# Kernel tuning notes

Measured on AMD Instinct MI355X. Metric: run time of the kernel, lower is better.

Reference implementation:

```python
import jax, jax.numpy as jnp
import numpy as np

T, B, IN_S, H, OUT_S = 2048, 4096, 1, 20, 1


def setup_inputs() -> dict:
    key = jax.random.key(0)
    k_u, k_ih, k_hh, k_out = jax.random.split(key, 4)
    s = 1.0 / np.sqrt(H)  # PyTorch-style uniform init scale (values only; math identical)
    return {
        "u": jax.random.normal(k_u, (T, B, IN_S), dtype=jnp.float32),
        "W_ih": jax.random.uniform(k_ih, (4 * H, IN_S), minval=-s, maxval=s, dtype=jnp.float32),
        "W_hh": jax.random.uniform(k_hh, (4 * H, H), minval=-s, maxval=s, dtype=jnp.float32),
        "W_out": jax.random.uniform(k_out, (OUT_S, H), minval=-s, maxval=s, dtype=jnp.float32),
    }


def _lstm(u, W_ih, W_hh):
    # u: [T, B, IN_S]; PyTorch gate order: i, f, g, o. No biases (bias=False).
    Tn, Bn, _ = u.shape
    # Precompute input projections for all timesteps at once: [T, B, 4H]
    x_proj = jnp.einsum("tbi,gi->tbg", u, W_ih)

    def step(carry, xg):
        h, c = carry  # [B, H] each
        gates = xg + h @ W_hh.T  # [B, 4H]
        i, f, g, o = jnp.split(gates, 4, axis=-1)
        i = jax.nn.sigmoid(i)
        f = jax.nn.sigmoid(f)
        g = jnp.tanh(g)
        o = jax.nn.sigmoid(o)
        c = f * c + i * g
        h = o * jnp.tanh(c)
        return (h, c), h

    h0 = jnp.zeros((Bn, W_hh.shape[1]), dtype=u.dtype)
    c0 = jnp.zeros_like(h0)
    (_, _), ys = jax.lax.scan(step, (h0, c0), x_proj)
    return ys  # [T, B, H]


def reference(u, W_ih, W_hh, W_out):
    ys = _lstm(u, W_ih, W_hh)          # [T, B, H]
    return jnp.einsum("tbh,oh->tbo", ys, W_out)  # [T, B, OUT_S]
```

## Files before the change

### kernel.cpp

```cpp
#include <hip/hip_runtime.h>
#include <hip/hip_bf16.h>
#include <math.h>

#define TT 2048
#define BB 4096
#define HH 20

typedef float v2f __attribute__((ext_vector_type(2)));

#define L2E 1.4426950408889634f

__device__ __forceinline__ float rcp_fast(float x)  { return __builtin_amdgcn_rcpf(x); }
__device__ __forceinline__ float exp2_fast(float x) { return __builtin_amdgcn_exp2f(x); }

__device__ __forceinline__ v2f pk_fma(v2f a, v2f b, v2f c) {
    return __builtin_elementwise_fma(a, b, c);
}
__device__ __forceinline__ v2f exp2v(v2f x) { v2f r; r.x = exp2_fast(x.x); r.y = exp2_fast(x.y); return r; }
__device__ __forceinline__ v2f rcpv(v2f x)  { v2f r; r.x = rcp_fast(x.x);  r.y = rcp_fast(x.y);  return r; }
__device__ __forceinline__ v2f absv(v2f x)  { v2f r; r.x = fabsf(x.x);     r.y = fabsf(x.y);     return r; }
__device__ __forceinline__ v2f csignv(v2f x, v2f s) {
    v2f r; r.x = copysignf(x.x, s.x); r.y = copysignf(x.y, s.y); return r;
}

__global__ __launch_bounds__(64, 1) void lstm_fused_kernel(
    const float* __restrict__ u,
    const float* __restrict__ W_ih,
    const float* __restrict__ W_hh,
    const float* __restrict__ W_out,
    float* __restrict__ y)
{
    __shared__ __align__(16) float hbuf[128];

    const int lane = threadIdx.x;
    int q, wa, jbase;
    bool is_y = false;
    if (lane < 40) {
        q = lane / 10;
        const int p = lane - q * 10;
        wa = q * HH + 2 * p;
        jbase = 2 * p;
    } else {
        is_y = (lane < 44);
        q = is_y ? (lane - 40) : 0;
        wa = 4 * HH + (lane - 40) * 2;
        jbase = 0;
    }

    for (int i = lane; i < 128; i += 64) hbuf[i] = 0.0f;
    asm volatile("" ::: "memory");

    v2f wgv[4][2][10];
    v2f wihv[4][2];
    const float gsc[4] = {-L2E, -L2E, -2.0f * L2E, -L2E};
    #pragma unroll
    for (int g = 0; g < 4; ++g) {
        #pragma unroll
        for (int r = 0; r < 2; ++r) {
            const int row = g * HH + jbase + r;
            #pragma unroll
            for (int m = 0; m < 10; ++m) {
                wgv[g][r][m].x = gsc[g] * W_hh[row * HH + 2 * m];
                wgv[g][r][m].y = gsc[g] * W_hh[row * HH + 2 * m + 1];
            }
            wihv[g][r].x = gsc[g] * W_ih[row];
            wihv[g][r].y = 0.0f;
        }
    }
    if (lane >= 40) {
        #pragma unroll
        for (int m = 0; m < 10; ++m) {
            wgv[0][0][m].x = W_out[2 * m];
            wgv[0][0][m].y = W_out[2 * m + 1];
        }
        wihv[0][0].x = 0.0f;
    }

    const v2f* hs = (const v2f*)&hbuf[q * HH];
    v2f* hw = (v2f*)&hbuf[wa];

    v2f cv = {0.0f, 0.0f};
    const float* __restrict__ up = u + (size_t)blockIdx.x * 4 + q;
    float* yp = y + (size_t)blockIdx.x * 4 + (lane - 40);

    float u_cur[8];
    #pragma unroll
    for (int k = 0; k < 8; ++k) u_cur[k] = up[(size_t)k * BB];

    const v2f one = {1.0f, 1.0f};
    const v2f n2l2e = {-2.0f * L2E, -2.0f * L2E};

    for (int t8 = 0; t8 < TT; t8 += 8) {
        #pragma unroll
        for (int g = 0; g < 4; ++g) {
            #pragma unroll
            for (int r = 0; r < 2; ++r) {
                #pragma unroll
                for (int m = 0; m < 10; ++m)
                    asm volatile("" : "+v"(wgv[g][r][m].x), "+v"(wgv[g][r][m].y));
                asm volatile("" : "+v"(wihv[g][r].x));
            }
        }

        const int tn = (t8 + 8 < TT) ? (t8 + 8) : t8;
        float u_nxt[8];
        #pragma unroll
        for (int k = 0; k < 8; ++k) u_nxt[k] = up[(size_t)(tn + k) * BB];

        float y8[8];

        #pragma unroll
        for (int tt = 0; tt < 8; ++tt) {
            v2f h2[10];
            #pragma unroll
            for (int m = 0; m < 10; ++m) h2[m] = hs[m];

            const float uv = u_cur[tt];
            const v2f uv2 = {uv, uv};
            v2f a[4][2];
            #pragma unroll
            for (int g = 0; g < 4; ++g) {
                #pragma unroll
                for (int r = 0; r < 2; ++r) a[g][r] = wihv[g][r] * uv2;
            }

            #pragma unroll
            for (int m = 0; m < 10; ++m) {
                const v2f hp = h2[m];
                a[2][0] = pk_fma(wgv[2][0][m], hp, a[2][0]);
                a[2][1] = pk_fma(wgv[2][1][m], hp, a[2][1]);
                a[1][0] = pk_fma(wgv[1][0][m], hp, a[1][0]);
                a[1][1] = pk_fma(wgv[1][1][m], hp, a[1][1]);
                a[0][0] = pk_fma(wgv[0][0][m], hp, a[0][0]);
                a[0][1] = pk_fma(wgv[0][1][m], hp, a[0][1]);
                a[3][0] = pk_fma(wgv[3][0][m], hp, a[3][0]);
                a[3][1] = pk_fma(wgv[3][1][m], hp, a[3][1]);
            }
            v2f gi, gf, gg, go;
            gi.x = a[0][0].x + a[0][0].y;  gi.y = a[0][1].x + a[0][1].y;
            gf.x = a[1][0].x + a[1][0].y;  gf.y = a[1][1].x + a[1][1].y;
            gg.x = a[2][0].x + a[2][0].y;  gg.y = a[2][1].x + a[2][1].y;
            go.x = a[3][0].x + a[3][0].y;  go.y = a[3][1].x + a[3][1].y;
            y8[tt] = gi.x;

            const v2f eg = exp2v(gg);
            const v2f ef = exp2v(gf);
            const v2f ei = exp2v(gi);
            const v2f eo = exp2v(go);
            const v2f pg = one + eg, pf = one + ef, pi2 = one + ei, po = one + eo;
            const v2f mg = one - eg;

            const v2f m1  = pg * pi2;
            const v2f num = pk_fma(cv, m1, mg * pf);
            const v2f rv  = rcpv(pf * m1);
            cv = num * rv;
            const v2f kn  = absv(num) * n2l2e;
            const v2f ec  = exp2v(kn * rv);
            const v2f pc  = one + ec;
            const v2f mcs = csignv(one - ec, num);
            const v2f hv  = mcs * rcpv(po * pc);

            *hw = hv;
        }

        if (is_y) {
            #pragma unroll
            for (int k = 0; k < 8; ++k) {
                const int idx = t8 - 1 + k;
                if (idx >= 0) yp[(size_t)idx * BB] = y8[k];
            }
        }

        #pragma unroll
        for (int k = 0; k < 8; ++k) u_cur[k] = u_nxt[k];
    }

    {
        v2f ay = {0.0f, 0.0f};
        #pragma unroll
        for (int m = 0; m < 10; ++m) ay = pk_fma(wgv[0][0][m], hs[m], ay);
        if (is_y) yp[(size_t)(TT - 1) * BB] = ay.x + ay.y;
    }
}

extern "C" void kernel_launch(void* const* d_in, const int* in_sizes, int n_in,
                              void* d_out, int out_size, void* d_ws, size_t ws_size,
                              hipStream_t stream) {
    const float* u     = (const float*)d_in[0];
    const float* W_ih  = (const float*)d_in[1];
    const float* W_hh  = (const float*)d_in[2];
    const float* W_out = (const float*)d_in[3];
    float* y = (float*)d_out;

    const int blocks = BB / 4;
    lstm_fused_kernel<<<dim3(blocks), dim3(64), 0, stream>>>(u, W_ih, W_hh, W_out, y);
}
```

Before: 742.6 us.

## Interleave two independent batch groups per wavefront to hide recurrence latency

Each 64-lane block now advances two independent groups of four batch elements (A and B) through the same timesteps, using the shared register-resident weights. The grid is halved to compensate. The goal is to hide the latency of the serial chain (LDS read, FMA, exp, reciprocal) by giving the scheduler a second independent chain to interleave within one wave. In exchange, half as many waves occupy the GPU's SIMDs, each wave needs more registers for the extra accumulators and hidden-state copies, and the unroll depth per load batch drops from 8 to 4 timesteps. The asm register-pinning barriers are also removed.

```diff
diff --git a/kernel.cpp b/kernel.cpp
--- a/kernel.cpp
+++ b/kernel.cpp
@@ -30,24 +30,27 @@
     const float* __restrict__ W_out,
     float* __restrict__ y)
 {
-    __shared__ __align__(16) float hbuf[128];
+    __shared__ __align__(16) float hbuf[224];
 
     const int lane = threadIdx.x;
-    int q, wa, jbase;
-    bool is_y = false;
+    int q = 0, jbase = 0, waA, waB;
+    bool is_yA = false, is_yB = false;
     if (lane < 40) {
         q = lane / 10;
         const int p = lane - q * 10;
-        wa = q * HH + 2 * p;
         jbase = 2 * p;
+        waA = q * HH + 2 * p;
+        waB = 80 + q * HH + 2 * p;
     } else {
-        is_y = (lane < 44);
-        q = is_y ? (lane - 40) : 0;
-        wa = 4 * HH + (lane - 40) * 2;
-        jbase = 0;
-    }
-
-    for (int i = lane; i < 128; i += 64) hbuf[i] = 0.0f;
+        is_yA = (lane < 44);
+        is_yB = (lane >= 44) && (lane < 48);
+        waA = 160 + (lane - 40) * 2;
+        waB = 160 + (lane - 40) * 2;
+    }
+    const int rbA = is_yA ? (lane - 40) * HH : (lane < 40 ? q * HH : 0);
+    const int rbB = 80 + (is_yB ? (lane - 44) * HH : (lane < 40 ? q * HH : 0));
+
+    for (int i = lane; i < 224; i += 64) hbuf[i] = 0.0f;
     asm volatile("" ::: "memory");
 
     v2f wgv[4][2][10];
@@ -76,110 +79,165 @@
         wihv[0][0].x = 0.0f;
     }
 
-    const v2f* hs = (const v2f*)&hbuf[q * HH];
-    v2f* hw = (v2f*)&hbuf[wa];
-
-    v2f cv = {0.0f, 0.0f};
-    const float* __restrict__ up = u + (size_t)blockIdx.x * 4 + q;
-    float* yp = y + (size_t)blockIdx.x * 4 + (lane - 40);
-
-    float u_cur[8];
+    const v2f* hsA = (const v2f*)&hbuf[rbA];
+    const v2f* hsB = (const v2f*)&hbuf[rbB];
+    v2f* hwA = (v2f*)&hbuf[waA];
+    v2f* hwB = (v2f*)&hbuf[waB];
+
+    v2f cvA = {0.0f, 0.0f}, cvB = {0.0f, 0.0f};
+    const size_t base = (size_t)blockIdx.x * 8;
+    const float* upA = u + base + (lane < 40 ? q : 0);
+    const float* upB = u + base + 4 + (lane < 40 ? q : 0);
+    float* ypA = y + base + (lane - 40);
+    float* ypB = y + base + 4 + (lane - 44);
+
+    float u_curA[4], u_curB[4];
     #pragma unroll
-    for (int k = 0; k < 8; ++k) u_cur[k] = up[(size_t)k * BB];
+    for (int k = 0; k < 4; ++k) { u_curA[k] = upA[(size_t)k * BB]; u_curB[k] = upB[(size_t)k * BB]; }
 
     const v2f one = {1.0f, 1.0f};
     const v2f n2l2e = {-2.0f * L2E, -2.0f * L2E};
 
-    for (int t8 = 0; t8 < TT; t8 += 8) {
-        #pragma unroll
-        for (int g = 0; g < 4; ++g) {
-            #pragma unroll
-            for (int r = 0; r < 2; ++r) {
-                #pragma unroll
-                for (int m = 0; m < 10; ++m)
-                    asm volatile("" : "+v"(wgv[g][r][m].x), "+v"(wgv[g][r][m].y));
-                asm volatile("" : "+v"(wihv[g][r].x));
-            }
-        }
-
-        const int tn = (t8 + 8 < TT) ? (t8 + 8) : t8;
-        float u_nxt[8];
-        #pragma unroll
-        for (int k = 0; k < 8; ++k) u_nxt[k] = up[(size_t)(tn + k) * BB];
-
-        float y8[8];
-
-        #pragma unroll
-        for (int tt = 0; tt < 8; ++tt) {
-            v2f h2[10];
-            #pragma unroll
-            for (int m = 0; m < 10; ++m) h2[m] = hs[m];
-
-            const float uv = u_cur[tt];
-            const v2f uv2 = {uv, uv};
-            v2f a[4][2];
+    for (int t4 = 0; t4 < TT; t4 += 4) {
+        const int tn = (t4 + 4 < TT) ? (t4 + 4) : t4;
+        float u_nxtA[4], u_nxtB[4];
+        #pragma unroll
+        for (int k = 0; k < 4; ++k) {
+            u_nxtA[k] = upA[(size_t)(tn + k) * BB];
+            u_nxtB[k] = upB[(size_t)(tn + k) * BB];
+        }
+
+        float y4A[4], y4B[4];
+
+        #pragma unroll
+        for (int tt = 0; tt < 4; ++tt) {
+            v2f h2A[10], h2B[10];
+            #pragma unroll
+            for (int m = 0; m < 10; ++m) h2A[m] = hsA[m];
+            #pragma unroll
+            for (int m = 0; m < 10; ++m) h2B[m] = hsB[m];
+
+            const float uvA = u_curA[tt];
+            const float uvB = u_curB[tt];
+            const v2f uv2A = {uvA, uvA};
+            const v2f uv2B = {uvB, uvB};
+            v2f aA[4][2], aB[4][2];
             #pragma unroll
             for (int g = 0; g < 4; ++g) {
                 #pragma unroll
-                for (int r = 0; r < 2; ++r) a[g][r] = wihv[g][r] * uv2;
+                for (int r = 0; r < 2; ++r) {
+                    aA[g][r] = wihv[g][r] * uv2A;
+                    aB[g][r] = wihv[g][r] * uv2B;
+                }
             }
 
             #pragma unroll
             for (int m = 0; m < 10; ++m) {
-                const v2f hp = h2[m];
-                a[2][0] = pk_fma(wgv[2][0][m], hp, a[2][0]);
-                a[2][1] = pk_fma(wgv[2][1][m], hp, a[2][1]);
-                a[1][0] = pk_fma(wgv[1][0][m], hp, a[1][0]);
-                a[1][1] = pk_fma(wgv[1][1][m], hp, a[1][1]);
-                a[0][0] = pk_fma(wgv[0][0][m], hp, a[0][0]);
-                a[0][1] = pk_fma(wgv[0][1][m], hp, a[0][1]);
-                a[3][0] = pk_fma(wgv[3][0][m], hp, a[3][0]);
-                a[3][1] = pk_fma(wgv[3][1][m], hp, a[3][1]);
-            }
-            v2f gi, gf, gg, go;
-            gi.x = a[0][0].x + a[0][0].y;  gi.y = a[0][1].x + a[0][1].y;
-            gf.x = a[1][0].x + a[1][0].y;  gf.y = a[1][1].x + a[1][1].y;
-            gg.x = a[2][0].x + a[2][0].y;  gg.y = a[2][1].x + a[2][1].y;
-            go.x = a[3][0].x + a[3][0].y;  go.y = a[3][1].x + a[3][1].y;
-            y8[tt] = gi.x;
-
-            const v2f eg = exp2v(gg);
-            const v2f ef = exp2v(gf);
-            const v2f ei = exp2v(gi);
-            const v2f eo = exp2v(go);
-            const v2f pg = one + eg, pf = one + ef, pi2 = one + ei, po = one + eo;
-            const v2f mg = one - eg;
-
-            const v2f m1  = pg * pi2;
-            const v2f num = pk_fma(cv, m1, mg * pf);
-            const v2f rv  = rcpv(pf * m1);
-            cv = num * rv;
-            const v2f kn  = absv(num) * n2l2e;
-            const v2f ec  = exp2v(kn * rv);
-            const v2f pc  = one + ec;
-            const v2f mcs = csignv(one - ec, num);
-            const v2f hv  = mcs * rcpv(po * pc);
-
-            *hw = hv;
-        }
-
-        if (is_y) {
-            #pragma unroll
-            for (int k = 0; k < 8; ++k) {
-                const int idx = t8 - 1 + k;
-                if (idx >= 0) yp[(size_t)idx * BB] = y8[k];
-            }
-        }
-
-        #pragma unroll
-        for (int k = 0; k < 8; ++k) u_cur[k] = u_nxt[k];
+                const v2f hp = h2A[m];
+                aA[2][0] = pk_fma(wgv[2][0][m], hp, aA[2][0]);
+                aA[2][1] = pk_fma(wgv[2][1][m], hp, aA[2][1]);
+                aA[1][0] = pk_fma(wgv[1][0][m], hp, aA[1][0]);
+                aA[1][1] = pk_fma(wgv[1][1][m], hp, aA[1][1]);
+                aA[0][0] = pk_fma(wgv[0][0][m], hp, aA[0][0]);
+                aA[0][1] = pk_fma(wgv[0][1][m], hp, aA[0][1]);
+                aA[3][0] = pk_fma(wgv[3][0][m], hp, aA[3][0]);
+                aA[3][1] = pk_fma(wgv[3][1][m], hp, aA[3][1]);
+            }
+            #pragma unroll
+            for (int m = 0; m < 10; ++m) {
+                const v2f hp = h2B[m];
+                aB[2][0] = pk_fma(wgv[2][0][m], hp, aB[2][0]);
+                aB[2][1] = pk_fma(wgv[2][1][m], hp, aB[2][1]);
+                aB[1][0] = pk_fma(wgv[1][0][m], hp, aB[1][0]);
+                aB[1][1] = pk_fma(wgv[1][1][m], hp, aB[1][1]);
+                aB[0][0] = pk_fma(wgv[0][0][m], hp, aB[0][0]);
+                aB[0][1] = pk_fma(wgv[0][1][m], hp, aB[0][1]);
+                aB[3][0] = pk_fma(wgv[3][0][m], hp, aB[3][0]);
+                aB[3][1] = pk_fma(wgv[3][1][m], hp, aB[3][1]);
+            }
+
+            {
+                v2f gi, gf, gg, go;
+                gi.x = aA[0][0].x + aA[0][0].y;  gi.y = aA[0][1].x + aA[0][1].y;
+                gf.x = aA[1][0].x + aA[1][0].y;  gf.y = aA[1][1].x + aA[1][1].y;
+                gg.x = aA[2][0].x + aA[2][0].y;  gg.y = aA[2][1].x + aA[2][1].y;
+                go.x = aA[3][0].x + aA[3][0].y;  go.y = aA[3][1].x + aA[3][1].y;
+                y4A[tt] = gi.x;
+
+                const v2f eg = exp2v(gg);
+                const v2f ef = exp2v(gf);
+                const v2f ei = exp2v(gi);
+                const v2f eo = exp2v(go);
+                const v2f pg = one + eg, pf = one + ef, pi2 = one + ei, po = one + eo;
+                const v2f mg = one - eg;
+
+                const v2f m1  = pg * pi2;
+                const v2f num = pk_fma(cvA, m1, mg * pf);
+                const v2f rv  = rcpv(pf * m1);
+                cvA = num * rv;
+                const v2f kn  = absv(num) * n2l2e;
+                const v2f ec  = exp2v(kn * rv);
+                const v2f pc  = one + ec;
+                const v2f mcs = csignv(one - ec, num);
+                const v2f hv  = mcs * rcpv(po * pc);
+                *hwA = hv;
+            }
+            {
+                v2f gi, gf, gg, go;
+                gi.x = aB[0][0].x + aB[0][0].y;  gi.y = aB[0][1].x + aB[0][1].y;
+                gf.x = aB[1][0].x + aB[1][0].y;  gf.y = aB[1][1].x + aB[1][1].y;
+                gg.x = aB[2][0].x + aB[2][0].y;  gg.y = aB[2][1].x + aB[2][1].y;
+                go.x = aB[3][0].x + aB[3][0].y;  go.y = aB[3][1].x + aB[3][1].y;
+                y4B[tt] = gi.x;
+
+                const v2f eg = exp2v(gg);
+                const v2f ef = exp2v(gf);
+                const v2f ei = exp2v(gi);
+                const v2f eo = exp2v(go);
+                const v2f pg = one + eg, pf = one + ef, pi2 = one + ei, po = one + eo;
+                const v2f mg = one - eg;
+
+                const v2f m1  = pg * pi2;
+                const v2f num = pk_fma(cvB, m1, mg * pf);
+                const v2f rv  = rcpv(pf * m1);
+                cvB = num * rv;
+                const v2f kn  = absv(num) * n2l2e;
+                const v2f ec  = exp2v(kn * rv);
+                const v2f pc  = one + ec;
+                const v2f mcs = csignv(one - ec, num);
+                const v2f hv  = mcs * rcpv(po * pc);
+                *hwB = hv;
+            }
+        }
+
+        if (is_yA) {
+            #pragma unroll
+            for (int k = 0; k < 4; ++k) {
+                const int idx = t4 - 1 + k;
+                if (idx >= 0) ypA[(size_t)idx * BB] = y4A[k];
+            }
+        }
+        if (is_yB) {
+            #pragma unroll
+            for (int k = 0; k < 4; ++k) {
+                const int idx = t4 - 1 + k;
+                if (idx >= 0) ypB[(size_t)idx * BB] = y4B[k];
+            }
+        }
+
+        #pragma unroll
+        for (int k = 0; k < 4; ++k) { u_curA[k] = u_nxtA[k]; u_curB[k] = u_nxtB[k]; }
     }
 
     {
-        v2f ay = {0.0f, 0.0f};
-        #pragma unroll
-        for (int m = 0; m < 10; ++m) ay = pk_fma(wgv[0][0][m], hs[m], ay);
-        if (is_y) yp[(size_t)(TT - 1) * BB] = ay.x + ay.y;
+        v2f ayA = {0.0f, 0.0f}, ayB = {0.0f, 0.0f};
+        #pragma unroll
+        for (int m = 0; m < 10; ++m) {
+            ayA = pk_fma(wgv[0][0][m], hsA[m], ayA);
+            ayB = pk_fma(wgv[0][0][m], hsB[m], ayB);
+        }
+        if (is_yA) ypA[(size_t)(TT - 1) * BB] = ayA.x + ayA.y;
+        if (is_yB) ypB[(size_t)(TT - 1) * BB] = ayB.x + ayB.y;
     }
 }
 
@@ -192,6 +250,6 @@
     const float* W_out = (const float*)d_in[3];
     float* y = (float*)d_out;
 
-    const int blocks = BB / 4;
+    const int blocks = BB / 8;
     lstm_fused_kernel<<<dim3(blocks), dim3(64), 0, stream>>>(u, W_ih, W_hh, W_out, y);
 }
```

Result: slower. 1.514 ms (+103.8%).
